# Performance work log

Measured on AMD Instinct MI355X. Metric: run time of the kernel, lower is better.

The kernel has to match this reference:

```python
import jax, jax.numpy as jnp
import numpy as np


def setup_inputs() -> dict:
    key = jax.random.key(0)
    kq, kk, kv = jax.random.split(key, 3)
    B, H, S, D = 2, 8, 4096, 64
    return {
        "query": jax.random.normal(kq, (B, H, S, D), dtype=jnp.float32),
        "key": jax.random.normal(kk, (B, H, S, D), dtype=jnp.float32),
        "value": jax.random.normal(kv, (B, H, S, D), dtype=jnp.float32),
    }


def reference(query, key, value):
    # NOTE: the torch source overwrites sqrt(d) with d, so the divisor is D, not sqrt(D).
    d = query.shape[-1]
    # score: [B, H, S_q, S_k]
    score = jnp.einsum("bhqd,bhkd->bhqk", query, key) / d
    relu = jax.nn.relu(score)  # no softmax / row normalization
    out = jnp.einsum("bhqk,bhkd->bhqd", relu, value)
    return out
```

## Files before the change

### kernel.cpp

```cpp
#include <hip/hip_runtime.h>
#include <hip/hip_bf16.h>
#include <stdint.h>


#define NH 16
#define SEQ 4096
#define DD 64
#define HE (SEQ*DD)
#define HB (HE*2)
#define Q16_OFF 0
#define K16_OFF (NH*HB)
#define V16_OFF (2*NH*HB)
#define WS_NEED (3*NH*HB)

typedef __attribute__((ext_vector_type(8)))  short    bf16x8;
typedef __attribute__((ext_vector_type(16))) float    f32x16;
typedef __attribute__((ext_vector_type(4)))  uint32_t u32x4;

__device__ inline uint32_t f2bf1(float f) {
  return (uint32_t)__builtin_bit_cast(unsigned short, __float2bfloat16(f));
}
__device__ inline uint32_t pack2bf(float a, float b) {
  return f2bf1(a) | (f2bf1(b) << 16);
}
__device__ inline uint32_t relu2(uint32_t w) {
  uint32_t r;
  asm("v_pk_max_f16 %0, %1, 0" : "=v"(r) : "v"(w));
  return r;
}

__global__ __launch_bounds__(256) void prepass_kernel(const float* __restrict__ Q,
                                                      const float* __restrict__ K,
                                                      const float* __restrict__ V,
                                                      char* __restrict__ ws) {
  __shared__ float vt[64*65];
  int bx = blockIdx.x, tid = threadIdx.x;
  if (bx < 2048) {
    size_t base = ((size_t)bx*256 + tid)*8;
    const float4* s = (const float4*)(Q + base);
    float4 a = s[0], b = s[1];
    const float sc = 1.0f/64.0f;
    u32x4 o;
    o.x = pack2bf(a.x*sc, a.y*sc);
    o.y = pack2bf(a.z*sc, a.w*sc);
    o.z = pack2bf(b.x*sc, b.y*sc);
    o.w = pack2bf(b.z*sc, b.w*sc);
    *(u32x4*)(ws + Q16_OFF + base*2) = o;
  } else if (bx < 3072) {
    int tile = bx - 2048;
    int head = tile >> 6, t = tile & 63;
    int r = tid >> 2, c0 = (tid & 3) * 16;
    const float4* s4 = (const float4*)(K + (size_t)head*HE + ((size_t)(t*64 + r))*64 + c0);
    float4 f0 = s4[0], f1 = s4[1], f2 = s4[2], f3 = s4[3];
    u32x4 c_lo, c_hi;
    c_lo.x = pack2bf(f0.x, f0.y); c_lo.y = pack2bf(f0.z, f0.w);
    c_lo.z = pack2bf(f1.x, f1.y); c_lo.w = pack2bf(f1.z, f1.w);
    c_hi.x = pack2bf(f2.x, f2.y); c_hi.y = pack2bf(f2.z, f2.w);
    c_hi.z = pack2bf(f3.x, f3.y); c_hi.w = pack2bf(f3.z, f3.w);
    char* tb = ws + K16_OFF + ((size_t)head*64 + t)*8192;
    int sw = (r & 7) << 4;
    *(u32x4*)(tb + r*128 + ((c0*2)      ^ sw)) = c_lo;
    *(u32x4*)(tb + r*128 + ((c0*2 + 16) ^ sw)) = c_hi;
  } else {
    int tile = bx - 3072;
    int head = tile >> 6, t = tile & 63;
    int k = tid >> 2, c0 = (tid & 3)*16;
    const float4* s4 = (const float4*)(V + (size_t)head*HE + ((size_t)(t*64 + k))*64 + c0);
    float4 f0 = s4[0], f1 = s4[1], f2 = s4[2], f3 = s4[3];
    float tmp[16] = {f0.x,f0.y,f0.z,f0.w, f1.x,f1.y,f1.z,f1.w,
                     f2.x,f2.y,f2.z,f2.w, f3.x,f3.y,f3.z,f3.w};
    #pragma unroll
    for (int j = 0; j < 16; ++j) vt[k*65 + c0 + j] = tmp[j];
    __syncthreads();
    int d = tid >> 2, k0 = (tid & 3)*16;
    float v2[16];
    #pragma unroll
    for (int j = 0; j < 16; ++j) v2[j] = vt[(k0 + j)*65 + d];
    u32x4 c_lo, c_hi;
    c_lo.x = pack2bf(v2[0],  v2[1]);  c_lo.y = pack2bf(v2[2],  v2[3]);
    c_lo.z = pack2bf(v2[4],  v2[5]);  c_lo.w = pack2bf(v2[6],  v2[7]);
    c_hi.x = pack2bf(v2[8],  v2[9]);  c_hi.y = pack2bf(v2[10], v2[11]);
    c_hi.z = pack2bf(v2[12], v2[13]); c_hi.w = pack2bf(v2[14], v2[15]);
    char* tb = ws + V16_OFF + ((size_t)head*64 + t)*8192;
    int sw = (d & 7) << 4;
    *(u32x4*)(tb + d*128 + ((k0*2)      ^ sw)) = c_lo;
    *(u32x4*)(tb + d*128 + ((k0*2 + 16) ^ sw)) = c_hi;
  }
}

__global__ __launch_bounds__(256, 2) void attn_kernel(const char* __restrict__ ws,
                                                      float* __restrict__ out) {
  __shared__ __align__(16) char lds[8*8192];
  int bx = blockIdx.x;
  int head = bx >> 5, qblk = bx & 31;
  int tid = threadIdx.x;
  int lane = tid & 63, w = tid >> 6;
  int l31 = lane & 31, h = lane >> 5;
  int g  = w >> 1;
  int mq = w & 1;

  const char* q16 = ws + Q16_OFF + (size_t)head*HB;
  const char* k16 = ws + K16_OFF + (size_t)head*HB;
  const char* v16 = ws + V16_OFF + (size_t)head*HB;
  int qrow0 = qblk*128 + mq*64;

  bf16x8 qf[2][4];
  #pragma unroll
  for (int m = 0; m < 2; ++m)
    #pragma unroll
    for (int t = 0; t < 4; ++t)
      qf[m][t] = *(const bf16x8*)(q16 + ((size_t)(qrow0 + m*32 + l31)*64 + t*16 + h*8)*2);

  f32x16 kZero;
  #pragma unroll
  for (int i = 0; i < 16; ++i) kZero[i] = 0.f;

  f32x16 o[2][2];
  #pragma unroll
  for (int m = 0; m < 2; ++m)
    #pragma unroll
    for (int nd = 0; nd < 2; ++nd)
      #pragma unroll
      for (int i = 0; i < 16; ++i) o[m][nd][i] = 0.f;

  char* ldsg = lds + g*4*8192;

  auto stage = [&](int cur, int kt) {
    const char* ktile = k16 + (size_t)(g*32 + kt)*8192;
    const char* vtile = v16 + (size_t)(g*32 + kt)*8192;
    char* lk = ldsg + (cur*2 + 0)*8192;
    char* lv = ldsg + (cur*2 + 1)*8192;
    #pragma unroll
    for (int c = 0; c < 4; ++c) {
      int off = (mq*4 + c)*1024;
      __builtin_amdgcn_global_load_lds(
          (const __attribute__((address_space(1))) void*)(ktile + off + lane*16),
          (__attribute__((address_space(3))) void*)(lk + off), 16, 0, 0);
      __builtin_amdgcn_global_load_lds(
          (const __attribute__((address_space(1))) void*)(vtile + off + lane*16),
          (__attribute__((address_space(3))) void*)(lv + off), 16, 0, 0);
    }
  };

  auto compute = [&](int cur) {
    const char* lk = ldsg + (cur*2 + 0)*8192;
    const char* lv = ldsg + (cur*2 + 1)*8192;
    f32x16 st[2][2];
    #pragma unroll
    for (int n = 0; n < 2; ++n) {
      bf16x8 kf[4];
      int row = n*32 + l31;
      int sw = (row & 7) << 4;
      #pragma unroll
      for (int t = 0; t < 4; ++t)
        kf[t] = *(const bf16x8*)(lk + row*128 + ((t*32 + h*16) ^ sw));
      __builtin_amdgcn_s_setprio(1);
      #pragma unroll
      for (int m = 0; m < 2; ++m) {
        f32x16 acc = __builtin_amdgcn_mfma_f32_32x32x16_bf16(kf[0], qf[m][0], kZero, 0, 0, 0);
        #pragma unroll
        for (int t = 1; t < 4; ++t)
          acc = __builtin_amdgcn_mfma_f32_32x32x16_bf16(kf[t], qf[m][t], acc, 0, 0, 0);
        st[m][n] = acc;
      }
      __builtin_amdgcn_s_setprio(0);
    }
    bf16x8 pa[2][4];
    #pragma unroll
    for (int m = 0; m < 2; ++m)
      #pragma unroll
      for (int n = 0; n < 2; ++n)
        #pragma unroll
        for (int kn = 0; kn < 2; ++kn) {
          uint32_t a0 = pack2bf(st[m][n][kn*8+0], st[m][n][kn*8+1]);
          uint32_t b0 = pack2bf(st[m][n][kn*8+2], st[m][n][kn*8+3]);
          uint32_t a2 = pack2bf(st[m][n][kn*8+4], st[m][n][kn*8+5]);
          uint32_t b2 = pack2bf(st[m][n][kn*8+6], st[m][n][kn*8+7]);
          asm("v_permlane32_swap_b32 %0, %1" : "+v"(a0), "+v"(a2));
          asm("v_permlane32_swap_b32 %0, %1" : "+v"(b0), "+v"(b2));
          union { uint32_t u[4]; bf16x8 v; } pk;
          pk.u[0] = relu2(a0);
          pk.u[1] = relu2(b0);
          pk.u[2] = relu2(a2);
          pk.u[3] = relu2(b2);
          pa[m][n*2 + kn] = pk.v;
        }
    bf16x8 vf[2][4];
    #pragma unroll
    for (int nd = 0; nd < 2; ++nd) {
      int row = nd*32 + l31;
      int sw = (row & 7) << 4;
      #pragma unroll
      for (int ks = 0; ks < 4; ++ks)
        vf[nd][ks] = *(const bf16x8*)(lv + row*128 + ((ks*32 + h*16) ^ sw));
    }
    __builtin_amdgcn_s_setprio(1);
    #pragma unroll
    for (int m = 0; m < 2; ++m)
      #pragma unroll
      for (int nd = 0; nd < 2; ++nd)
        #pragma unroll
        for (int ks = 0; ks < 4; ++ks)
          o[m][nd] = __builtin_amdgcn_mfma_f32_32x32x16_bf16(pa[m][ks], vf[nd][ks], o[m][nd], 0, 0, 0);
    __builtin_amdgcn_s_setprio(0);
  };

  stage(0, 0);
  __syncthreads();
  #pragma unroll 1
  for (int kt = 0; kt < 32; ++kt) {
    int cur = kt & 1;
    if (kt + 1 < 32) stage(cur ^ 1, kt + 1);
    compute(cur);
    __syncthreads();
  }

  float* red = (float*)lds;
  if (g == 1) {
    #pragma unroll
    for (int m = 0; m < 2; ++m)
      #pragma unroll
      for (int nd = 0; nd < 2; ++nd)
        #pragma unroll
        for (int r = 0; r < 16; ++r) {
          int ql = m*32 + (r & 3) + 8*(r >> 2) + 4*h;
          red[mq*4096 + ql*64 + nd*32 + l31] = o[m][nd][r];
        }
  }
  __syncthreads();
  if (g == 0) {
    float* outh = out + (size_t)head*HE;
    #pragma unroll
    for (int m = 0; m < 2; ++m)
      #pragma unroll
      for (int nd = 0; nd < 2; ++nd)
        #pragma unroll
        for (int r = 0; r < 16; ++r) {
          int ql = m*32 + (r & 3) + 8*(r >> 2) + 4*h;
          float v = o[m][nd][r] + red[mq*4096 + ql*64 + nd*32 + l31];
          outh[(size_t)(qrow0 + ql)*64 + nd*32 + l31] = v;
        }
  }
}

extern "C" void kernel_launch(void* const* d_in, const int* in_sizes, int n_in,
                              void* d_out, int out_size, void* d_ws, size_t ws_size,
                              hipStream_t stream) {
  if (n_in < 3 || ws_size < (size_t)WS_NEED) return;
  const float* Q = (const float*)d_in[0];
  const float* K = (const float*)d_in[1];
  const float* V = (const float*)d_in[2];
  float* out = (float*)d_out;
  char* ws = (char*)d_ws;
  hipLaunchKernelGGL(prepass_kernel, dim3(4096), dim3(256), 0, stream, Q, K, V, ws);
  hipLaunchKernelGGL(attn_kernel,    dim3(512),  dim3(256), 0, stream, ws, out);
}
```

Measured before the change: 87.81 us.

## Pre-swizzle K/V/Q into MFMA fragment layout and load directly from global

The prepass now writes Q, K and V in per-lane MFMA fragment order, so the attention kernel reads its operands straight from global memory (through L2) into registers. This removes the LDS staging, the double buffering and the per-iteration __syncthreads, leaving only an occasional s_barrier to keep the waves loosely in step. It also remaps block IDs so that neighbouring blocks spread across heads, intended for better L2/XCD locality, and uses v_cvt_pk_bf16_f32 for packing. The risk is that global-load latency is no longer hidden behind a prefetch, and K/V are refetched per wave pair.

```diff
diff --git a/kernel.cpp b/kernel.cpp
--- a/kernel.cpp
+++ b/kernel.cpp
@@ -23,6 +23,11 @@
 __device__ inline uint32_t pack2bf(float a, float b) {
   return f2bf1(a) | (f2bf1(b) << 16);
 }
+__device__ inline uint32_t cvtpk(float lo, float hi) {
+  uint32_t r;
+  asm("v_cvt_pk_bf16_f32 %0, %1, %2" : "=v"(r) : "v"(lo), "v"(hi));
+  return r;
+}
 __device__ inline uint32_t relu2(uint32_t w) {
   uint32_t r;
   asm("v_pk_max_f16 %0, %1, 0" : "=v"(r) : "v"(w));
@@ -36,8 +41,9 @@
   __shared__ float vt[64*65];
   int bx = blockIdx.x, tid = threadIdx.x;
   if (bx < 2048) {
-    size_t base = ((size_t)bx*256 + tid)*8;
-    const float4* s = (const float4*)(Q + base);
+    int head = bx >> 7, qg = bx & 127;
+    int r31 = tid & 31, c = tid >> 5;
+    const float4* s = (const float4*)(Q + (size_t)head*HE + ((size_t)(qg*32 + r31))*64 + c*8);
     float4 a = s[0], b = s[1];
     const float sc = 1.0f/64.0f;
     u32x4 o;
@@ -45,7 +51,8 @@
     o.y = pack2bf(a.z*sc, a.w*sc);
     o.z = pack2bf(b.x*sc, b.y*sc);
     o.w = pack2bf(b.z*sc, b.w*sc);
-    *(u32x4*)(ws + Q16_OFF + base*2) = o;
+    char* tb = ws + Q16_OFF + (size_t)head*HB;
+    *(u32x4*)(tb + ((qg*4 + (c >> 1))*1024) + ((c & 1)*32 + r31)*16) = o;
   } else if (bx < 3072) {
     int tile = bx - 2048;
     int head = tile >> 6, t = tile & 63;
@@ -58,9 +65,9 @@
     c_hi.x = pack2bf(f2.x, f2.y); c_hi.y = pack2bf(f2.z, f2.w);
     c_hi.z = pack2bf(f3.x, f3.y); c_hi.w = pack2bf(f3.z, f3.w);
     char* tb = ws + K16_OFF + ((size_t)head*64 + t)*8192;
-    int sw = (r & 7) << 4;
-    *(u32x4*)(tb + r*128 + ((c0*2)      ^ sw)) = c_lo;
-    *(u32x4*)(tb + r*128 + ((c0*2 + 16) ^ sw)) = c_hi;
+    char* chunk = tb + ((r >> 5)*4 + (tid & 3))*1024 + (r & 31)*16;
+    *(u32x4*)(chunk)       = c_lo;
+    *(u32x4*)(chunk + 512) = c_hi;
   } else {
     int tile = bx - 3072;
     int head = tile >> 6, t = tile & 63;
@@ -82,34 +89,35 @@
     c_hi.x = pack2bf(v2[8],  v2[9]);  c_hi.y = pack2bf(v2[10], v2[11]);
     c_hi.z = pack2bf(v2[12], v2[13]); c_hi.w = pack2bf(v2[14], v2[15]);
     char* tb = ws + V16_OFF + ((size_t)head*64 + t)*8192;
-    int sw = (d & 7) << 4;
-    *(u32x4*)(tb + d*128 + ((k0*2)      ^ sw)) = c_lo;
-    *(u32x4*)(tb + d*128 + ((k0*2 + 16) ^ sw)) = c_hi;
+    char* chunk = tb + ((d >> 5)*4 + (tid & 3))*1024 + (d & 31)*16;
+    *(u32x4*)(chunk)       = c_lo;
+    *(u32x4*)(chunk + 512) = c_hi;
   }
 }
 
 __global__ __launch_bounds__(256, 2) void attn_kernel(const char* __restrict__ ws,
                                                       float* __restrict__ out) {
-  __shared__ __align__(16) char lds[8*8192];
-  int bx = blockIdx.x;
+  __shared__ float red[128*64];
+  int bid = blockIdx.x;
+  int bx = (bid & 7) * 64 + (bid >> 3);
   int head = bx >> 5, qblk = bx & 31;
   int tid = threadIdx.x;
   int lane = tid & 63, w = tid >> 6;
   int l31 = lane & 31, h = lane >> 5;
   int g  = w >> 1;
-  int mq = w & 1;
-
-  const char* q16 = ws + Q16_OFF + (size_t)head*HB;
-  const char* k16 = ws + K16_OFF + (size_t)head*HB;
-  const char* v16 = ws + V16_OFF + (size_t)head*HB;
-  int qrow0 = qblk*128 + mq*64;
-
+  int wg = w & 1;
+
+  const char* q16   = ws + Q16_OFF + (size_t)head*HB;
+  const char* kbase = ws + K16_OFF + (size_t)head*HB + (size_t)g*32*8192;
+  const char* vbase = ws + V16_OFF + (size_t)head*HB + (size_t)g*32*8192;
+
+  int qg0 = qblk*4 + wg*2;
   bf16x8 qf[2][4];
   #pragma unroll
   for (int m = 0; m < 2; ++m)
     #pragma unroll
     for (int t = 0; t < 4; ++t)
-      qf[m][t] = *(const bf16x8*)(q16 + ((size_t)(qrow0 + m*32 + l31)*64 + t*16 + h*8)*2);
+      qf[m][t] = *(const bf16x8*)(q16 + ((size_t)((qg0 + m)*4 + t))*1024 + lane*16);
 
   f32x16 kZero;
   #pragma unroll
@@ -123,48 +131,33 @@
       #pragma unroll
       for (int i = 0; i < 16; ++i) o[m][nd][i] = 0.f;
 
-  char* ldsg = lds + g*4*8192;
-
-  auto stage = [&](int cur, int kt) {
-    const char* ktile = k16 + (size_t)(g*32 + kt)*8192;
-    const char* vtile = v16 + (size_t)(g*32 + kt)*8192;
-    char* lk = ldsg + (cur*2 + 0)*8192;
-    char* lv = ldsg + (cur*2 + 1)*8192;
-    #pragma unroll
-    for (int c = 0; c < 4; ++c) {
-      int off = (mq*4 + c)*1024;
-      __builtin_amdgcn_global_load_lds(
-          (const __attribute__((address_space(1))) void*)(ktile + off + lane*16),
-          (__attribute__((address_space(3))) void*)(lk + off), 16, 0, 0);
-      __builtin_amdgcn_global_load_lds(
-          (const __attribute__((address_space(1))) void*)(vtile + off + lane*16),
-          (__attribute__((address_space(3))) void*)(lv + off), 16, 0, 0);
-    }
-  };
-
-  auto compute = [&](int cur) {
-    const char* lk = ldsg + (cur*2 + 0)*8192;
-    const char* lv = ldsg + (cur*2 + 1)*8192;
+  #pragma unroll 1
+  for (int kt = 0; kt < 32; ++kt) {
+    const char* kp = kbase + (size_t)kt*8192;
+    const char* vp = vbase + (size_t)kt*8192;
+    bf16x8 kf[2][4], vf[2][4];
+    #pragma unroll
+    for (int i = 0; i < 8; ++i)
+      kf[i >> 2][i & 3] = *(const bf16x8*)(kp + i*1024 + lane*16);
+    #pragma unroll
+    for (int i = 0; i < 8; ++i)
+      vf[i >> 2][i & 3] = *(const bf16x8*)(vp + i*1024 + lane*16);
+
     f32x16 st[2][2];
     #pragma unroll
     for (int n = 0; n < 2; ++n) {
-      bf16x8 kf[4];
-      int row = n*32 + l31;
-      int sw = (row & 7) << 4;
-      #pragma unroll
-      for (int t = 0; t < 4; ++t)
-        kf[t] = *(const bf16x8*)(lk + row*128 + ((t*32 + h*16) ^ sw));
       __builtin_amdgcn_s_setprio(1);
       #pragma unroll
       for (int m = 0; m < 2; ++m) {
-        f32x16 acc = __builtin_amdgcn_mfma_f32_32x32x16_bf16(kf[0], qf[m][0], kZero, 0, 0, 0);
+        f32x16 acc = __builtin_amdgcn_mfma_f32_32x32x16_bf16(kf[n][0], qf[m][0], kZero, 0, 0, 0);
         #pragma unroll
         for (int t = 1; t < 4; ++t)
-          acc = __builtin_amdgcn_mfma_f32_32x32x16_bf16(kf[t], qf[m][t], acc, 0, 0, 0);
+          acc = __builtin_amdgcn_mfma_f32_32x32x16_bf16(kf[n][t], qf[m][t], acc, 0, 0, 0);
         st[m][n] = acc;
       }
       __builtin_amdgcn_s_setprio(0);
     }
+
     bf16x8 pa[2][4];
     #pragma unroll
     for (int m = 0; m < 2; ++m)
@@ -172,28 +165,20 @@
       for (int n = 0; n < 2; ++n)
         #pragma unroll
         for (int kn = 0; kn < 2; ++kn) {
-          uint32_t a0 = pack2bf(st[m][n][kn*8+0], st[m][n][kn*8+1]);
-          uint32_t b0 = pack2bf(st[m][n][kn*8+2], st[m][n][kn*8+3]);
-          uint32_t a2 = pack2bf(st[m][n][kn*8+4], st[m][n][kn*8+5]);
-          uint32_t b2 = pack2bf(st[m][n][kn*8+6], st[m][n][kn*8+7]);
-          asm("v_permlane32_swap_b32 %0, %1" : "+v"(a0), "+v"(a2));
-          asm("v_permlane32_swap_b32 %0, %1" : "+v"(b0), "+v"(b2));
+          uint32_t w0 = cvtpk(st[m][n][kn*8+0], st[m][n][kn*8+1]);
+          uint32_t w1 = cvtpk(st[m][n][kn*8+2], st[m][n][kn*8+3]);
+          uint32_t w2 = cvtpk(st[m][n][kn*8+4], st[m][n][kn*8+5]);
+          uint32_t w3 = cvtpk(st[m][n][kn*8+6], st[m][n][kn*8+7]);
+          asm("v_permlane32_swap_b32 %0, %1" : "+v"(w0), "+v"(w2));
+          asm("v_permlane32_swap_b32 %0, %1" : "+v"(w1), "+v"(w3));
           union { uint32_t u[4]; bf16x8 v; } pk;
-          pk.u[0] = relu2(a0);
-          pk.u[1] = relu2(b0);
-          pk.u[2] = relu2(a2);
-          pk.u[3] = relu2(b2);
+          pk.u[0] = relu2(w0);
+          pk.u[1] = relu2(w1);
+          pk.u[2] = relu2(w2);
+          pk.u[3] = relu2(w3);
           pa[m][n*2 + kn] = pk.v;
         }
-    bf16x8 vf[2][4];
-    #pragma unroll
-    for (int nd = 0; nd < 2; ++nd) {
-      int row = nd*32 + l31;
-      int sw = (row & 7) << 4;
-      #pragma unroll
-      for (int ks = 0; ks < 4; ++ks)
-        vf[nd][ks] = *(const bf16x8*)(lv + row*128 + ((ks*32 + h*16) ^ sw));
-    }
+
     __builtin_amdgcn_s_setprio(1);
     #pragma unroll
     for (int m = 0; m < 2; ++m)
@@ -203,19 +188,11 @@
         for (int ks = 0; ks < 4; ++ks)
           o[m][nd] = __builtin_amdgcn_mfma_f32_32x32x16_bf16(pa[m][ks], vf[nd][ks], o[m][nd], 0, 0, 0);
     __builtin_amdgcn_s_setprio(0);
-  };
-
-  stage(0, 0);
+
+    if ((kt & 7) == 7) __builtin_amdgcn_s_barrier();
+  }
+
   __syncthreads();
-  #pragma unroll 1
-  for (int kt = 0; kt < 32; ++kt) {
-    int cur = kt & 1;
-    if (kt + 1 < 32) stage(cur ^ 1, kt + 1);
-    compute(cur);
-    __syncthreads();
-  }
-
-  float* red = (float*)lds;
   if (g == 1) {
     #pragma unroll
     for (int m = 0; m < 2; ++m)
@@ -223,8 +200,8 @@
       for (int nd = 0; nd < 2; ++nd)
         #pragma unroll
         for (int r = 0; r < 16; ++r) {
-          int ql = m*32 + (r & 3) + 8*(r >> 2) + 4*h;
-          red[mq*4096 + ql*64 + nd*32 + l31] = o[m][nd][r];
+          int ql = wg*64 + m*32 + (r & 3) + 8*(r >> 2) + 4*h;
+          red[ql*64 + nd*32 + l31] = o[m][nd][r];
         }
   }
   __syncthreads();
@@ -236,9 +213,9 @@
       for (int nd = 0; nd < 2; ++nd)
         #pragma unroll
         for (int r = 0; r < 16; ++r) {
-          int ql = m*32 + (r & 3) + 8*(r >> 2) + 4*h;
-          float v = o[m][nd][r] + red[mq*4096 + ql*64 + nd*32 + l31];
-          outh[(size_t)(qrow0 + ql)*64 + nd*32 + l31] = v;
+          int ql = wg*64 + m*32 + (r & 3) + 8*(r >> 2) + 4*h;
+          float v = o[m][nd][r] + red[ql*64 + nd*32 + l31];
+          outh[(size_t)(qblk*128 + ql)*64 + nd*32 + l31] = v;
         }
   }
 }
```

New measurement: 81.54 us. 1.08x faster.
